# Kernel tuning notes

Hardware: AMD Instinct MI355X
Metric: run time of the kernel (lower is better)

## Reference

```python
import jax, jax.numpy as jnp
import numpy as np

B, N, C, H, W = 2, 6, 64, 28, 50
D = 59  # len(arange(1.0, 60.0, 1.0))
BH, BW = 200, 200
BEV_X0, BEV_Y0 = -50.0, -50.0
RES_X, RES_Y = 0.5, 0.5  # (50-(-50))/200


def setup_inputs() -> dict:
    key = jax.random.key(0)
    k1, k2 = jax.random.split(key)
    features = jax.random.normal(k1, (B, N, C, H, W), dtype=jnp.float32)
    # depth distribution over D bins (softmax-normalized, as a depth net would emit)
    depth = jax.nn.softmax(jax.random.normal(k2, (B, N, D, H, W), dtype=jnp.float32), axis=2)
    # realistic pinhole intrinsics for a WxH feature map
    K = np.zeros((B, N, 3, 3), np.float32)
    K[..., 0, 0] = float(W)
    K[..., 1, 1] = float(W)
    K[..., 0, 2] = W / 2.0
    K[..., 1, 2] = H / 2.0
    K[..., 2, 2] = 1.0
    # cam-to-ego extrinsics: axis remap (z_cam->x_ego, x_cam->-y_ego, y_cam->-z_ego)
    # composed with a per-camera yaw, plus a small mounting translation
    R0 = np.array([[0, 0, 1], [-1, 0, 0], [0, -1, 0]], np.float32)
    E = np.zeros((B, N, 4, 4), np.float32)
    for n in range(N):
        yaw = 2.0 * np.pi * n / N
        Rz = np.array([[np.cos(yaw), -np.sin(yaw), 0.0],
                       [np.sin(yaw), np.cos(yaw), 0.0],
                       [0.0, 0.0, 1.0]], np.float32)
        E[:, n, :3, :3] = Rz @ R0
        E[:, n, 0, 3] = 1.5 * np.cos(yaw)
        E[:, n, 1, 3] = 1.5 * np.sin(yaw)
        E[:, n, 2, 3] = 1.6
    E[..., 3, 3] = 1.0
    return {
        "features": features,
        "depth": depth,
        "intrinsics": jnp.asarray(K),
        "extrinsics": jnp.asarray(E),
    }


def _frustum_ego(intrinsics, extrinsics):
    # pixel grid (H, W, 3) homogeneous coords
    xs = jnp.linspace(0.0, W - 1.0, W, dtype=jnp.float32)
    ys = jnp.linspace(0.0, H - 1.0, H, dtype=jnp.float32)
    yy, xx = jnp.meshgrid(ys, xs, indexing="ij")
    pix = jnp.stack([xx, yy, jnp.ones_like(xx)], axis=-1)  # (H, W, 3)
    depth_bins = jnp.arange(1.0, 60.0, 1.0, dtype=jnp.float32)  # (D,)
    frustum_cam = pix[None] * depth_bins[:, None, None, None]  # (D, H, W, 3)
    K_inv = jnp.linalg.inv(intrinsics)  # (B, N, 3, 3)
    cam = jnp.einsum("bnij,dhwj->bndhwi", K_inv, frustum_cam)  # (B, N, D, H, W, 3)
    R = extrinsics[..., :3, :3]
    t = extrinsics[..., :3, 3]
    ego = jnp.einsum("bnij,bndhwj->bndhwi", R, cam) + t[:, :, None, None, None, :]
    return ego


def reference(features, depth, intrinsics, extrinsics):
    ego = _frustum_ego(intrinsics, extrinsics)  # (B, N, D, H, W, 3)

    # lift: outer product of features (B,N,C,H,W) and depth (B,N,D,H,W)
    lifted = features[:, :, None] * depth[:, :, :, None]  # (B, N, D, C, H, W)
    lifted = lifted.transpose(0, 1, 2, 4, 5, 3).reshape(B, -1, C)  # b (n d h w) c

    fr = ego.reshape(B, -1, 3)  # b (n d h w) xyz
    x, y, z = fr[..., 0], fr[..., 1], fr[..., 2]
    # torch .long() truncates toward zero -> astype(int32) matches
    bx = ((x - BEV_X0) / RES_X).astype(jnp.int32)
    by = ((y - BEV_Y0) / RES_Y).astype(jnp.int32)
    valid = (bx >= 0) & (bx < BW) & (by >= 0) & (by < BH) & (z > 0)

    # flat scatter index with per-batch offset; invalid -> dummy segment (dropped)
    b_off = (jnp.arange(B, dtype=jnp.int32) * (BH * BW))[:, None]
    flat_idx = jnp.where(valid, b_off + by * BW + bx, B * BH * BW)
    seg = jax.ops.segment_sum(
        lifted.reshape(-1, C), flat_idx.reshape(-1), num_segments=B * BH * BW + 1
    )
    bev = seg[: B * BH * BW].reshape(B, BH, BW, C).transpose(0, 3, 1, 2)  # (B, C, BH, BW)
    return bev
```

## Files before the change

kernel.cpp:

```cpp
#include <hip/hip_runtime.h>
#include <hip/hip_bf16.h>

#define Bc 2
#define Nc 6
#define Cc 64
#define Hc 28
#define Wc 50
#define Dc 59
#define BHc 200
#define BWc 200

__global__ __launch_bounds__(256) void fp_scatter2(
    const float* __restrict__ feats,
    const float* __restrict__ depth,
    const float* __restrict__ Kmat,
    const float* __restrict__ Emat,
    float* __restrict__ acc)
{
    __shared__ float feat_lds[Hc][Cc];
    __shared__ float dep_lds[Dc][Hc];

    int blk = blockIdx.x;
    int w  = blk % Wc;
    int bn = blk / Wc;
    int b  = bn / Nc;
    int tid  = threadIdx.x;
    int lane = tid & 63;
    int wid  = tid >> 6;

    const size_t HW = (size_t)Hc * Wc;
    const float* fbase = feats + (size_t)bn * Cc * HW + w;
    const float* dbase = depth + (size_t)bn * Dc * HW + w;

    for (int h = wid; h < Hc; h += 4)
        feat_lds[h][lane] = fbase[(size_t)lane * HW + (size_t)h * Wc];
    for (int idx = tid; idx < Dc * Hc; idx += 256) {
        int d = idx / Hc, h = idx % Hc;
        dep_lds[d][h] = dbase[(size_t)d * HW + (size_t)h * Wc];
    }

    const float* K = Kmat + (size_t)bn * 9;
    float k00 = K[0], k01 = K[1], k02 = K[2];
    float k10 = K[3], k11 = K[4], k12 = K[5];
    float k20 = K[6], k21 = K[7], k22 = K[8];

    float c00 = __fsub_rn(__fmul_rn(k11, k22), __fmul_rn(k12, k21));
    float c01 = __fsub_rn(__fmul_rn(k12, k20), __fmul_rn(k10, k22));
    float c02 = __fsub_rn(__fmul_rn(k10, k21), __fmul_rn(k11, k20));
    float det = __fadd_rn(__fadd_rn(__fmul_rn(k00, c00), __fmul_rn(k01, c01)),
                          __fmul_rn(k02, c02));
    float i00 = __fdiv_rn(c00, det);
    float i01 = __fdiv_rn(__fsub_rn(__fmul_rn(k02, k21), __fmul_rn(k01, k22)), det);
    float i02 = __fdiv_rn(__fsub_rn(__fmul_rn(k01, k12), __fmul_rn(k02, k11)), det);
    float i10 = __fdiv_rn(c01, det);
    float i11 = __fdiv_rn(__fsub_rn(__fmul_rn(k00, k22), __fmul_rn(k02, k20)), det);
    float i12 = __fdiv_rn(__fsub_rn(__fmul_rn(k02, k10), __fmul_rn(k00, k12)), det);
    float i20 = __fdiv_rn(c02, det);
    float i21 = __fdiv_rn(__fsub_rn(__fmul_rn(k01, k20), __fmul_rn(k00, k21)), det);
    float i22 = __fdiv_rn(__fsub_rn(__fmul_rn(k00, k11), __fmul_rn(k01, k10)), det);

    const float* E = Emat + (size_t)bn * 16;
    float r00 = E[0], r01 = E[1], r02 = E[2],  tx = E[3];
    float r10 = E[4], r11 = E[5], r12 = E[6],  ty = E[7];
    float r20 = E[8], r21 = E[9], r22 = E[10], tz = E[11];

    __syncthreads();

    float xf = (float)w;
    float* accb = acc + (size_t)b * (BHc * BWc) * Cc;

    for (int d = wid; d < Dc; d += 4) {
        float db = (float)(d + 1);

        int h = lane;
        float yf = (float)h;
        float px = __fmul_rn(xf, db);
        float py = __fmul_rn(yf, db);
        float pz = db;

        float cx = __fadd_rn(__fadd_rn(__fmul_rn(i00, px), __fmul_rn(i01, py)), __fmul_rn(i02, pz));
        float cy = __fadd_rn(__fadd_rn(__fmul_rn(i10, px), __fmul_rn(i11, py)), __fmul_rn(i12, pz));
        float cz = __fadd_rn(__fadd_rn(__fmul_rn(i20, px), __fmul_rn(i21, py)), __fmul_rn(i22, pz));

        float ex = __fadd_rn(__fadd_rn(__fadd_rn(__fmul_rn(r00, cx), __fmul_rn(r01, cy)), __fmul_rn(r02, cz)), tx);
        float ey = __fadd_rn(__fadd_rn(__fadd_rn(__fmul_rn(r10, cx), __fmul_rn(r11, cy)), __fmul_rn(r12, cz)), ty);
        float ez = __fadd_rn(__fadd_rn(__fadd_rn(__fmul_rn(r20, cx), __fmul_rn(r21, cy)), __fmul_rn(r22, cz)), tz);

        int bx = (int)(__fmul_rn(__fadd_rn(ex, 50.0f), 2.0f));
        int by = (int)(__fmul_rn(__fadd_rn(ey, 50.0f), 2.0f));

        bool valid = (h < Hc) & (bx >= 0) & (bx < BWc) & (by >= 0) & (by < BHc) & (ez > 0.0f);
        int binidx = by * BWc + bx;

        unsigned long long vm = __ballot(valid);
        if (vm == 0ULL) continue;

        int first = __builtin_ctzll(vm);
        int prim  = __shfl(binidx, first);
        unsigned long long match = __ballot(valid && (binidx == prim));
        unsigned long long rest  = vm & ~match;

        float accv = 0.0f;
        for (unsigned long long m = match; m; m &= (m - 1)) {
            int hh = __builtin_ctzll(m);
            accv = __fmaf_rn(feat_lds[hh][lane], dep_lds[d][hh], accv);
        }
        atomicAdd(&accb[(size_t)prim * Cc + lane], accv);

        while (rest) {
            int hh = __builtin_ctzll(rest);
            rest &= rest - 1;
            int bidx = __shfl(binidx, hh);
            atomicAdd(&accb[(size_t)bidx * Cc + lane],
                      __fmul_rn(feat_lds[hh][lane], dep_lds[d][hh]));
        }
    }
}

__global__ __launch_bounds__(256) void fp_transpose_kernel(
    const float* __restrict__ acc, float* __restrict__ out)
{
    __shared__ float tile[64][65];
    const int P = BHc * BWc;
    int b = blockIdx.y;
    int p0 = blockIdx.x * 64;
    int tx = threadIdx.x & 63;
    int ty = threadIdx.x >> 6;

    const float* src = acc + (size_t)b * P * Cc;
#pragma unroll
    for (int i = 0; i < 16; ++i) {
        int row = ty * 16 + i;
        tile[row][tx] = src[(size_t)(p0 + row) * Cc + tx];
    }
    __syncthreads();
    float* dst = out + (size_t)b * Cc * P;
#pragma unroll
    for (int i = 0; i < 16; ++i) {
        int c = ty * 16 + i;
        dst[(size_t)c * P + p0 + tx] = tile[tx][c];
    }
}

extern "C" void kernel_launch(void* const* d_in, const int* in_sizes, int n_in,
                              void* d_out, int out_size, void* d_ws, size_t ws_size,
                              hipStream_t stream) {
    const float* feats = (const float*)d_in[0];
    const float* depth = (const float*)d_in[1];
    const float* Kmat  = (const float*)d_in[2];
    const float* Emat  = (const float*)d_in[3];
    float* out = (float*)d_out;

    const size_t ACC_ELEMS = (size_t)Bc * BHc * BWc * Cc;
    const size_t ACC_BYTES = ACC_ELEMS * sizeof(float);
    float* acc = (float*)d_ws;

    hipMemsetAsync(acc, 0, ACC_BYTES, stream);

    const int NBLK = Bc * Nc * Wc;
    fp_scatter2<<<NBLK, 256, 0, stream>>>(feats, depth, Kmat, Emat, acc);

    fp_transpose_kernel<<<dim3((BHc * BWc) / 64, Bc), 256, 0, stream>>>(acc, out);
}
```

Before: 110.2 us.

## Split depth range across blocks and batch primary-bin accumulation via swizzled LDS

Each (b,n,w) column is now handled by two blocks, each covering half the depth bins, which doubles the grid. Depth values are read straight into registers instead of being staged whole in LDS. Each wave handles 8 depth bins: it first writes the masked depth weights of the primary-bin pixels into an XOR-swizzled LDS matrix, then accumulates all 8 bins in one unrolled loop over h using float4 reads. This replaces the serial ballot-driven accumulation loop and is meant to add parallelism and cut per-depth serialization. The costs are that features are loaded twice per column and register pressure rises.

```diff
diff --git a/kernel.cpp b/kernel.cpp
--- a/kernel.cpp
+++ b/kernel.cpp
@@ -10,19 +10,25 @@
 #define BHc 200
 #define BWc 200
 
-__global__ __launch_bounds__(256) void fp_scatter2(
+#define DSPLIT 2
+#define DCHUNK 32
+#define DWAVE 8
+
+__global__ __launch_bounds__(256) void fp_scatter3(
     const float* __restrict__ feats,
     const float* __restrict__ depth,
     const float* __restrict__ Kmat,
     const float* __restrict__ Emat,
     float* __restrict__ acc)
 {
-    __shared__ float feat_lds[Hc][Cc];
-    __shared__ float dep_lds[Dc][Hc];
-
-    int blk = blockIdx.x;
-    int w  = blk % Wc;
-    int bn = blk / Wc;
+    __shared__ __align__(16) float feat_lds[Hc][Cc];
+    __shared__ __align__(16) float mdep[Hc][DCHUNK];
+
+    int blk   = blockIdx.x;
+    int dhalf = blk & 1;
+    int pix   = blk >> 1;
+    int w  = pix % Wc;
+    int bn = pix / Wc;
     int b  = bn / Nc;
     int tid  = threadIdx.x;
     int lane = tid & 63;
@@ -34,10 +40,6 @@
 
     for (int h = wid; h < Hc; h += 4)
         feat_lds[h][lane] = fbase[(size_t)lane * HW + (size_t)h * Wc];
-    for (int idx = tid; idx < Dc * Hc; idx += 256) {
-        int d = idx / Hc, h = idx % Hc;
-        dep_lds[d][h] = dbase[(size_t)d * HW + (size_t)h * Wc];
-    }
 
     const float* K = Kmat + (size_t)bn * 9;
     float k00 = K[0], k01 = K[1], k02 = K[2];
@@ -66,54 +68,92 @@
 
     __syncthreads();
 
+    float* accb = acc + (size_t)b * (BHc * BWc) * Cc;
+
+    int h = lane;
     float xf = (float)w;
-    float* accb = acc + (size_t)b * (BHc * BWc) * Cc;
-
-    for (int d = wid; d < Dc; d += 4) {
-        float db = (float)(d + 1);
-
-        int h = lane;
-        float yf = (float)h;
-        float px = __fmul_rn(xf, db);
-        float py = __fmul_rn(yf, db);
-        float pz = db;
-
-        float cx = __fadd_rn(__fadd_rn(__fmul_rn(i00, px), __fmul_rn(i01, py)), __fmul_rn(i02, pz));
-        float cy = __fadd_rn(__fadd_rn(__fmul_rn(i10, px), __fmul_rn(i11, py)), __fmul_rn(i12, pz));
-        float cz = __fadd_rn(__fadd_rn(__fmul_rn(i20, px), __fmul_rn(i21, py)), __fmul_rn(i22, pz));
-
-        float ex = __fadd_rn(__fadd_rn(__fadd_rn(__fmul_rn(r00, cx), __fmul_rn(r01, cy)), __fmul_rn(r02, cz)), tx);
-        float ey = __fadd_rn(__fadd_rn(__fadd_rn(__fmul_rn(r10, cx), __fmul_rn(r11, cy)), __fmul_rn(r12, cz)), ty);
-        float ez = __fadd_rn(__fadd_rn(__fadd_rn(__fmul_rn(r20, cx), __fmul_rn(r21, cy)), __fmul_rn(r22, cz)), tz);
-
-        int bx = (int)(__fmul_rn(__fadd_rn(ex, 50.0f), 2.0f));
-        int by = (int)(__fmul_rn(__fadd_rn(ey, 50.0f), 2.0f));
-
-        bool valid = (h < Hc) & (bx >= 0) & (bx < BWc) & (by >= 0) & (by < BHc) & (ez > 0.0f);
-        int binidx = by * BWc + bx;
-
-        unsigned long long vm = __ballot(valid);
-        if (vm == 0ULL) continue;
-
-        int first = __builtin_ctzll(vm);
-        int prim  = __shfl(binidx, first);
-        unsigned long long match = __ballot(valid && (binidx == prim));
-        unsigned long long rest  = vm & ~match;
-
-        float accv = 0.0f;
-        for (unsigned long long m = match; m; m &= (m - 1)) {
-            int hh = __builtin_ctzll(m);
-            accv = __fmaf_rn(feat_lds[hh][lane], dep_lds[d][hh], accv);
+    float yf = (float)h;
+    int ld0 = wid * DWAVE;
+
+    float accv[DWAVE];
+    int   prim[DWAVE];
+
+#pragma unroll
+    for (int k = 0; k < DWAVE; ++k) {
+        accv[k] = 0.0f;
+        prim[k] = -1;
+        int ld = ld0 + k;
+        int dg = dhalf * DCHUNK + ld;
+        if (dg < Dc) {
+            float db = (float)(dg + 1);
+            float dep = 0.0f;
+            if (h < Hc) dep = dbase[(size_t)dg * HW + (size_t)h * Wc];
+
+            float px = __fmul_rn(xf, db);
+            float py = __fmul_rn(yf, db);
+            float pz = db;
+
+            float cx = __fadd_rn(__fadd_rn(__fmul_rn(i00, px), __fmul_rn(i01, py)), __fmul_rn(i02, pz));
+            float cy = __fadd_rn(__fadd_rn(__fmul_rn(i10, px), __fmul_rn(i11, py)), __fmul_rn(i12, pz));
+            float cz = __fadd_rn(__fadd_rn(__fmul_rn(i20, px), __fmul_rn(i21, py)), __fmul_rn(i22, pz));
+
+            float ex = __fadd_rn(__fadd_rn(__fadd_rn(__fmul_rn(r00, cx), __fmul_rn(r01, cy)), __fmul_rn(r02, cz)), tx);
+            float ey = __fadd_rn(__fadd_rn(__fadd_rn(__fmul_rn(r10, cx), __fmul_rn(r11, cy)), __fmul_rn(r12, cz)), ty);
+            float ez = __fadd_rn(__fadd_rn(__fadd_rn(__fmul_rn(r20, cx), __fmul_rn(r21, cy)), __fmul_rn(r22, cz)), tz);
+
+            int bx = (int)(__fmul_rn(__fadd_rn(ex, 50.0f), 2.0f));
+            int by = (int)(__fmul_rn(__fadd_rn(ey, 50.0f), 2.0f));
+
+            bool valid = (h < Hc) & (bx >= 0) & (bx < BWc) & (by >= 0) & (by < BHc) & (ez > 0.0f);
+            int binidx = by * BWc + bx;
+
+            unsigned long long vm = __ballot(valid);
+            float val = 0.0f;
+            if (vm != 0ULL) {
+                int first = __builtin_ctzll(vm);
+                int pr = __shfl(binidx, first);
+                unsigned long long match = __ballot(valid && (binidx == pr));
+                unsigned long long rest  = vm & ~match;
+                prim[k] = pr;
+                val = (valid && (binidx == pr)) ? dep : 0.0f;
+
+                while (rest) {
+                    int hh2 = __builtin_ctzll(rest);
+                    rest &= rest - 1;
+                    int   bidx = __shfl(binidx, hh2);
+                    float dv   = __shfl(dep, hh2);
+                    atomicAdd(&accb[(size_t)bidx * Cc + lane],
+                              __fmul_rn(feat_lds[hh2][lane], dv));
+                }
+            }
+            if (h < Hc) {
+                char* base = (char*)&mdep[h][0];
+                *(float*)(base + (((ld << 2) ^ ((h & 7) << 4)))) = val;
+            }
         }
-        atomicAdd(&accb[(size_t)prim * Cc + lane], accv);
-
-        while (rest) {
-            int hh = __builtin_ctzll(rest);
-            rest &= rest - 1;
-            int bidx = __shfl(binidx, hh);
-            atomicAdd(&accb[(size_t)bidx * Cc + lane],
-                      __fmul_rn(feat_lds[hh][lane], dep_lds[d][hh]));
-        }
+    }
+
+    int lb0 = ld0 >> 2;
+#pragma unroll
+    for (int hh = 0; hh < Hc; ++hh) {
+        float f = feat_lds[hh][lane];
+        const float4* rowp = (const float4*)&mdep[hh][0];
+        float4 v0 = rowp[(lb0 + 0) ^ (hh & 7)];
+        float4 v1 = rowp[(lb0 + 1) ^ (hh & 7)];
+        accv[0] = __builtin_fmaf(f, v0.x, accv[0]);
+        accv[1] = __builtin_fmaf(f, v0.y, accv[1]);
+        accv[2] = __builtin_fmaf(f, v0.z, accv[2]);
+        accv[3] = __builtin_fmaf(f, v0.w, accv[3]);
+        accv[4] = __builtin_fmaf(f, v1.x, accv[4]);
+        accv[5] = __builtin_fmaf(f, v1.y, accv[5]);
+        accv[6] = __builtin_fmaf(f, v1.z, accv[6]);
+        accv[7] = __builtin_fmaf(f, v1.w, accv[7]);
+    }
+
+#pragma unroll
+    for (int k = 0; k < DWAVE; ++k) {
+        if (prim[k] >= 0)
+            atomicAdd(&accb[(size_t)prim[k] * Cc + lane], accv[k]);
     }
 }
 
@@ -157,8 +197,8 @@
 
     hipMemsetAsync(acc, 0, ACC_BYTES, stream);
 
-    const int NBLK = Bc * Nc * Wc;
-    fp_scatter2<<<NBLK, 256, 0, stream>>>(feats, depth, Kmat, Emat, acc);
+    const int NBLK = Bc * Nc * Wc * DSPLIT;
+    fp_scatter3<<<NBLK, 256, 0, stream>>>(feats, depth, Kmat, Emat, acc);
 
     fp_transpose_kernel<<<dim3((BHc * BWc) / 64, Bc), 256, 0, stream>>>(acc, out);
 }
```

Result: slower. 118.6 us (+7.6%).
